# Optimization experiments

Hardware: AMD Instinct MI355X
Metric: run time of the kernel (lower is better)

The kernel has to match this reference:

```python
import jax, jax.numpy as jnp
import numpy as np


def setup_inputs() -> dict:
    key = jax.random.key(0)
    k1, k2, k3, k4 = jax.random.split(key, 4)
    B, S, E, H = 8, 2048, 1024, 64
    x = jax.random.normal(k1, (B, S, E), dtype=jnp.float32)
    # nn.Linear(E, H, bias=False) weight is (H, E); we store transposed (E, H)
    scale = 1.0 / np.sqrt(E)
    Wk = jax.random.normal(k2, (E, H), dtype=jnp.float32) * scale
    Wq = jax.random.normal(k3, (E, H), dtype=jnp.float32) * scale
    Wv = jax.random.normal(k4, (E, H), dtype=jnp.float32) * scale
    return {"x": x, "Wk": Wk, "Wq": Wq, "Wv": Wv}


def reference(x, Wk, Wq, Wv):
    # x: (B, S, E); projections: (B, S, H)
    k = x @ Wk
    q = x @ Wq
    v = x @ Wv
    H = k.shape[-1]
    # scores: (B, S, S) with 1/sqrt(H) scaling as in the torch code
    scores = jnp.einsum("bqh,bkh->bqk", q, k) * (H ** -0.5)
    S = x.shape[1]
    causal = jnp.triu(jnp.full((S, S), -jnp.inf, dtype=scores.dtype), k=1)
    wei = jax.nn.softmax(scores + causal, axis=-1)
    # dropout p=0.0 -> identity
    return jnp.einsum("bqk,bkh->bqh", wei, v)
```

## Files before the change

kernel.cpp:

```cpp
#include <hip/hip_runtime.h>
#include <hip/hip_bf16.h>

typedef unsigned short ushort_t;
typedef __attribute__((ext_vector_type(8))) short short8;
typedef __attribute__((ext_vector_type(4))) short short4v;
typedef __attribute__((ext_vector_type(4))) float f32x4;

__device__ __forceinline__ float bf2f(ushort_t u) {
    unsigned int x = ((unsigned int)u) << 16;
    float f; __builtin_memcpy(&f, &x, 4); return f;
}
__device__ __forceinline__ ushort_t f2bf(float f) {
    __hip_bfloat16 h = __float2bfloat16(f);
    ushort_t u; __builtin_memcpy(&u, &h, 2); return u;
}
__device__ __forceinline__ unsigned packbf2(float a, float b) {
    return (unsigned)f2bf(a) | ((unsigned)f2bf(b) << 16);
}

__device__ __forceinline__ void gload16(const void* g, void* l) {
    __builtin_amdgcn_global_load_lds(
        (const __attribute__((address_space(1))) unsigned int*)g,
        (__attribute__((address_space(3))) unsigned int*)l, 16, 0, 0);
}

constexpr int E  = 1024;
constexpr int Hd = 64;
constexpr int S  = 2048;
constexpr int ROWS = 8 * 2048;
constexpr int NTOT = 192;
constexpr int LSTA = 88;

__global__ __launch_bounds__(256)
void prep_wt(const float* __restrict__ Wk, const float* __restrict__ Wq,
             const float* __restrict__ Wv, ushort_t* __restrict__ WT)
{
    int idx = blockIdx.x * 256 + threadIdx.x;
    int n = idx >> 10;
    int kk = idx & 1023;
    const float* W = (n < 64) ? Wq : ((n < 128) ? Wk : Wv);
    int h = n & 63;
    WT[idx] = f2bf(W[kk * Hd + h]);
}

__global__ __launch_bounds__(256, 2)
void proj_v11(const float* __restrict__ x, const ushort_t* __restrict__ WT,
              ushort_t* __restrict__ qo, ushort_t* __restrict__ ko,
              ushort_t* __restrict__ vTo)
{
    __shared__ alignas(16) float    XS[2][32 * 64];
    __shared__ alignas(16) ushort_t WS[2][192 * 64];

    const int t    = threadIdx.x;
    const int w    = t >> 6;
    const int lane = t & 63;
    const int m    = lane & 15;
    const int g    = lane >> 4;
    const int rl   = m & 7;
    const int rb   = blockIdx.x * 32;

    f32x4 accq[2], acck[2], accv[2];
    #pragma unroll
    for (int j = 0; j < 2; ++j) {
        accq[j] = (f32x4){0.f, 0.f, 0.f, 0.f};
        acck[j] = (f32x4){0.f, 0.f, 0.f, 0.f};
        accv[j] = (f32x4){0.f, 0.f, 0.f, 0.f};
    }

    const int xrow0 = t >> 4;
    const int xrow1 = (256 + t) >> 4;
    const int xU0   = (t & 15) ^ (xrow0 & 7);
    const int xU1   = (t & 15) ^ (xrow1 & 7);
    const float* xs0 = x + (size_t)(rb + xrow0) * E + xU0 * 4;
    const float* xs1 = x + (size_t)(rb + xrow1) * E + xU1 * 4;

    const ushort_t* wsrc[6];
    #pragma unroll
    for (int j = 0; j < 6; ++j) {
        const int L    = j * 256 + t;
        const int wrow = L >> 3;
        const int wU   = (L & 7) ^ (wrow & 7);
        wsrc[j] = WT + (size_t)wrow * E + wU * 8;
    }

    int xiA[2][2], xiB[2][2];
    #pragma unroll
    for (int h = 0; h < 2; ++h)
        #pragma unroll
        for (int kt = 0; kt < 2; ++kt) {
            const int row = h * 16 + m;
            const int U   = kt * 8 + 2 * g;
            xiA[h][kt] = (row * 16 + (U ^ rl)) * 4;
            xiB[h][kt] = (row * 16 + ((U + 1) ^ rl)) * 4;
        }
    int wiq[2], wik[2], wiv[2];
    #pragma unroll
    for (int kt = 0; kt < 2; ++kt) {
        const int U = kt * 4 + g;
        wiq[kt] = ((      w * 16 + m) * 8 + (U ^ rl)) * 8;
        wik[kt] = ((64  + w * 16 + m) * 8 + (U ^ rl)) * 8;
        wiv[kt] = ((128 + w * 16 + m) * 8 + (U ^ rl)) * 8;
    }

    auto STAGE = [&](int buf, int c) {
        const int k0 = c * 64;
        char* xb = (char*)&XS[buf][0];
        char* wb = (char*)&WS[buf][0];
        gload16(xs0 + k0, xb + (size_t)t * 16);
        gload16(xs1 + k0, xb + (size_t)(256 + t) * 16);
        #pragma unroll
        for (int j = 0; j < 6; ++j)
            gload16(wsrc[j] + k0, wb + (size_t)(j * 256 + t) * 16);
    };

    auto COMPUTE = [&](int buf) {
        #pragma unroll
        for (int kt = 0; kt < 2; ++kt) {
            short8 fq = *(const short8*)&WS[buf][wiq[kt]];
            short8 fk = *(const short8*)&WS[buf][wik[kt]];
            short8 fv = *(const short8*)&WS[buf][wiv[kt]];
            #pragma unroll
            for (int h = 0; h < 2; ++h) {
                float4 A = *(const float4*)&XS[buf][xiA[h][kt]];
                float4 B = *(const float4*)&XS[buf][xiB[h][kt]];
                short8 a;
                {
                    unsigned u4[4];
                    u4[0] = packbf2(A.x, A.y);
                    u4[1] = packbf2(A.z, A.w);
                    u4[2] = packbf2(B.x, B.y);
                    u4[3] = packbf2(B.z, B.w);
                    __builtin_memcpy(&a, u4, 16);
                }
                accq[h] = __builtin_amdgcn_mfma_f32_16x16x32_bf16(a, fq, accq[h], 0, 0, 0);
                acck[h] = __builtin_amdgcn_mfma_f32_16x16x32_bf16(a, fk, acck[h], 0, 0, 0);
                accv[h] = __builtin_amdgcn_mfma_f32_16x16x32_bf16(fv, a, accv[h], 0, 0, 0);
            }
        }
    };

    STAGE(0, 0);
    __syncthreads();

    #pragma unroll 1
    for (int cc = 0; cc < 16; cc += 2) {
        STAGE(1, cc + 1);
        COMPUTE(0);
        __syncthreads();
        if (cc + 2 < 16) STAGE(0, cc + 2);
        COMPUTE(1);
        __syncthreads();
    }

    const int col   = w * 16 + m;
    const int batch = rb >> 11;
    const int seq0  = rb & (S - 1);
    #pragma unroll
    for (int mt = 0; mt < 2; ++mt) {
        const int orow = rb + mt * 16 + g * 4;
        #pragma unroll
        for (int r = 0; r < 4; ++r) {
            qo[(size_t)(orow + r) * Hd + col] = f2bf(accq[mt][r] * 0.125f);
            ko[(size_t)(orow + r) * Hd + col] = f2bf(acck[mt][r]);
        }
    }
    #pragma unroll
    for (int ns = 0; ns < 2; ++ns)
        #pragma unroll
        for (int r = 0; r < 4; ++r) {
            const int h = w * 16 + g * 4 + r;
            vTo[(size_t)batch * Hd * S + (size_t)h * S + seq0 + ns * 16 + m]
                = f2bf(accv[ns][r]);
        }
}

__global__ __launch_bounds__(256)
void attn_part(const ushort_t* __restrict__ q, const ushort_t* __restrict__ k,
               const ushort_t* __restrict__ vT,
               float* __restrict__ lp, ushort_t* __restrict__ op)
{
    const int bi     = blockIdx.x;
    const int parity = bi & 3;
    const int pr     = bi >> 2;
    const int batch  = pr & 7;
    const int tile   = 31 - (pr >> 3);
    const int qs0    = tile * 64;
    const int sidx   = (batch * 32 + tile) * 4 + parity;

    const ushort_t* kb  = k  + (size_t)batch * S * Hd;
    const ushort_t* vTb = vT + (size_t)batch * Hd * S;

    const int t    = threadIdx.x;
    const int w    = t >> 6;
    const int lane = t & 63;
    const int m    = lane & 15;
    const int g    = lane >> 4;

    __shared__ alignas(16) ushort_t KS [64][LSTA];
    __shared__ alignas(16) ushort_t VTS[64][LSTA];

    const ushort_t* qrow = q + (size_t)(batch * S + qs0 + w * 16 + m) * Hd;
    short8 qf0 = *(const short8*)(qrow + g * 8);
    short8 qf1 = *(const short8*)(qrow + 32 + g * 8);

    f32x4 o[4];
    #pragma unroll
    for (int j = 0; j < 4; ++j) o[j] = (f32x4){0.f, 0.f, 0.f, 0.f};
    float lrun = 0.f;
    const int qr = w * 16 + m;

    const int r1 = t >> 3, c16 = (t & 7) * 8;
    uint4 pk0, pk1, pv0, pv1;

    int c = parity;
    if (c <= tile) {
        const int key0 = c * 64;
        const ushort_t* kt_base = kb + (size_t)key0 * Hd;
        pk0 = *(const uint4*)(kt_base + t * 8);
        pk1 = *(const uint4*)(kt_base + (t + 256) * 8);
        pv0 = *(const uint4*)(vTb + (size_t)r1 * S + key0 + c16);
        pv1 = *(const uint4*)(vTb + (size_t)(r1 + 32) * S + key0 + c16);
    }

    for (; c <= tile; c += 4) {
        *(uint4*)&KS [r1][c16]       = pk0;
        *(uint4*)&KS [r1 + 32][c16]  = pk1;
        *(uint4*)&VTS[r1][c16]       = pv0;
        *(uint4*)&VTS[r1 + 32][c16]  = pv1;
        __syncthreads();

        if (c + 4 <= tile) {
            const int key0n = (c + 4) * 64;
            const ushort_t* kt_base = kb + (size_t)key0n * Hd;
            pk0 = *(const uint4*)(kt_base + t * 8);
            pk1 = *(const uint4*)(kt_base + (t + 256) * 8);
            pv0 = *(const uint4*)(vTb + (size_t)r1 * S + key0n + c16);
            pv1 = *(const uint4*)(vTb + (size_t)(r1 + 32) * S + key0n + c16);
        }

        f32x4 sacc[4];
        #pragma unroll
        for (int j = 0; j < 4; ++j) sacc[j] = (f32x4){0.f, 0.f, 0.f, 0.f};
        #pragma unroll
        for (int nt = 0; nt < 4; ++nt) {
            short8 b0 = *(const short8*)&KS[nt * 16 + m][g * 8];
            short8 b1 = *(const short8*)&KS[nt * 16 + m][32 + g * 8];
            sacc[nt] = __builtin_amdgcn_mfma_f32_16x16x32_bf16(b0, qf0, sacc[nt], 0, 0, 0);
            sacc[nt] = __builtin_amdgcn_mfma_f32_16x16x32_bf16(b1, qf1, sacc[nt], 0, 0, 0);
        }

        if (c == tile) {
            #pragma unroll
            for (int nt = 0; nt < 4; ++nt)
                #pragma unroll
                for (int r = 0; r < 4; ++r) {
                    const int keyl = nt * 16 + g * 4 + r;
                    sacc[nt][r] = (keyl > qr) ? 0.f : __expf(sacc[nt][r]);
                }
        } else {
            #pragma unroll
            for (int nt = 0; nt < 4; ++nt)
                #pragma unroll
                for (int r = 0; r < 4; ++r)
                    sacc[nt][r] = __expf(sacc[nt][r]);
        }

        #pragma unroll
        for (int nt = 0; nt < 4; ++nt)
            lrun += (sacc[nt][0] + sacc[nt][1]) + (sacc[nt][2] + sacc[nt][3]);

        unsigned pw0[4], pw1[4];
        #pragma unroll
        for (int s = 0; s < 4; ++s) {
            pw0[s] = packbf2(sacc[s][0], sacc[s][1]);
            pw1[s] = packbf2(sacc[s][2], sacc[s][3]);
        }

        #pragma unroll
        for (int s = 0; s < 4; ++s) {
            short4v pa;
            { unsigned u2[2] = {pw0[s], pw1[s]}; __builtin_memcpy(&pa, u2, 8); }
            #pragma unroll
            for (int nt = 0; nt < 4; ++nt) {
                short4v vb = *(const short4v*)&VTS[nt * 16 + m][s * 16 + g * 4];
                o[nt] = __builtin_amdgcn_mfma_f32_16x16x16bf16_1k(pa, vb, o[nt], 0, 0, 0);
            }
        }
        __syncthreads();
    }

    {
        float ts = lrun;
        ts += __shfl_xor(ts, 16, 64);
        ts += __shfl_xor(ts, 32, 64);
        if (lane < 16) lp[sidx * 64 + w * 16 + m] = ts;
    }
    #pragma unroll
    for (int nt = 0; nt < 4; ++nt)
        #pragma unroll
        for (int r = 0; r < 4; ++r)
            op[(size_t)sidx * 4096 + (w * 16 + g * 4 + r) * 64 + nt * 16 + m]
                = f2bf(o[nt][r]);
}

__global__ __launch_bounds__(256)
void attn_merge(const float* __restrict__ lp, const ushort_t* __restrict__ op,
                float* __restrict__ out)
{
    const int bq    = blockIdx.x;
    const int batch = bq >> 5;
    const int tile  = bq & 31;
    const int s0    = (batch * 32 + tile) * 4;

    const int t   = threadIdx.x;
    const int row = t >> 2;
    const int c16 = (t & 3) * 16;

    float l = 0.f;
    #pragma unroll
    for (int p = 0; p < 4; ++p) l += lp[(s0 + p) * 64 + row];
    const float inv = 1.f / l;

    float acc[16];
    #pragma unroll
    for (int j = 0; j < 16; ++j) acc[j] = 0.f;
    #pragma unroll
    for (int p = 0; p < 4; ++p) {
        short8 a0 = *(const short8*)(op + (size_t)(s0 + p) * 4096 + row * 64 + c16);
        short8 a1 = *(const short8*)(op + (size_t)(s0 + p) * 4096 + row * 64 + c16 + 8);
        #pragma unroll
        for (int j = 0; j < 8; ++j) {
            acc[j]     += bf2f((ushort_t)a0[j]);
            acc[j + 8] += bf2f((ushort_t)a1[j]);
        }
    }
    float* dst = out + (size_t)(batch * S + tile * 64 + row) * Hd + c16;
    #pragma unroll
    for (int j = 0; j < 16; ++j) dst[j] = acc[j] * inv;
}

extern "C" void kernel_launch(void* const* d_in, const int* in_sizes, int n_in,
                              void* d_out, int out_size, void* d_ws, size_t ws_size,
                              hipStream_t stream) {
    const float* x  = (const float*)d_in[0];
    const float* Wk = (const float*)d_in[1];
    const float* Wq = (const float*)d_in[2];
    const float* Wv = (const float*)d_in[3];
    float* out = (float*)d_out;

    ushort_t* qws  = (ushort_t*)d_ws;
    ushort_t* kws  = qws + (size_t)ROWS * Hd;
    ushort_t* vTws = kws + (size_t)ROWS * Hd;
    ushort_t* WT   = vTws + (size_t)ROWS * Hd;
    float*    lpp  = (float*)(WT + (size_t)NTOT * E);
    ushort_t* opp  = (ushort_t*)(lpp + 1024 * 64);

    prep_wt<<<(NTOT * E) / 256, 256, 0, stream>>>(Wk, Wq, Wv, WT);
    proj_v11<<<ROWS / 32, 256, 0, stream>>>(x, WT, qws, kws, vTws);
    attn_part<<<1024, 256, 0, stream>>>(qws, kws, vTws, lpp, opp);
    attn_merge<<<256, 256, 0, stream>>>(lpp, opp, out);
}
```

Measured before the change: 132.3 us.

## Enlarge projection tile to 64 rows with 512 threads and triple-buffered loads

The projection kernel now handles 64 rows per block with 8 waves, two row-halves sharing each weight tile, which halves the weight traffic per row. It also replaces double buffering with a three-stage pipeline using explicit vmcnt waits and raw barriers, so three chunks of loads stay in flight while compute runs. Shared memory grows to about 120 KB per block, which may limit residency to one block per CU. The hand-counted vmcnt values must match the five loads issued per stage.

```diff
diff --git a/kernel.cpp b/kernel.cpp
--- a/kernel.cpp
+++ b/kernel.cpp
@@ -30,6 +30,7 @@
 constexpr int ROWS = 8 * 2048;
 constexpr int NTOT = 192;
 constexpr int LSTA = 88;
+constexpr int BM   = 64;
 
 __global__ __launch_bounds__(256)
 void prep_wt(const float* __restrict__ Wk, const float* __restrict__ Wq,
@@ -43,13 +44,13 @@
     WT[idx] = f2bf(W[kk * Hd + h]);
 }
 
-__global__ __launch_bounds__(256, 2)
-void proj_v11(const float* __restrict__ x, const ushort_t* __restrict__ WT,
+__global__ __launch_bounds__(512, 2)
+void proj_v12(const float* __restrict__ x, const ushort_t* __restrict__ WT,
               ushort_t* __restrict__ qo, ushort_t* __restrict__ ko,
               ushort_t* __restrict__ vTo)
 {
-    __shared__ alignas(16) float    XS[2][32 * 64];
-    __shared__ alignas(16) ushort_t WS[2][192 * 64];
+    __shared__ alignas(16) float    XS[3][BM * 64];
+    __shared__ alignas(16) ushort_t WS[3][192 * 64];
 
     const int t    = threadIdx.x;
     const int w    = t >> 6;
@@ -57,7 +58,9 @@
     const int m    = lane & 15;
     const int g    = lane >> 4;
     const int rl   = m & 7;
-    const int rb   = blockIdx.x * 32;
+    const int cg   = w & 3;
+    const int mh   = w >> 2;
+    const int rb   = blockIdx.x * BM;
 
     f32x4 accq[2], acck[2], accv[2];
     #pragma unroll
@@ -67,20 +70,18 @@
         accv[j] = (f32x4){0.f, 0.f, 0.f, 0.f};
     }
 
-    const int xrow0 = t >> 4;
-    const int xrow1 = (256 + t) >> 4;
-    const int xU0   = (t & 15) ^ (xrow0 & 7);
-    const int xU1   = (t & 15) ^ (xrow1 & 7);
-    const float* xs0 = x + (size_t)(rb + xrow0) * E + xU0 * 4;
-    const float* xs1 = x + (size_t)(rb + xrow1) * E + xU1 * 4;
-
-    const ushort_t* wsrc[6];
-    #pragma unroll
-    for (int j = 0; j < 6; ++j) {
-        const int L    = j * 256 + t;
-        const int wrow = L >> 3;
-        const int wU   = (L & 7) ^ (wrow & 7);
-        wsrc[j] = WT + (size_t)wrow * E + wU * 8;
+    const int xr0 = t >> 4,         xu0 = (t & 15) ^ (xr0 & 7);
+    const int xr1 = (t + 512) >> 4, xu1 = (t & 15) ^ (xr1 & 7);
+    const float* xsrc0 = x + (size_t)(rb + xr0) * E + xu0 * 4;
+    const float* xsrc1 = x + (size_t)(rb + xr1) * E + xu1 * 4;
+
+    const ushort_t* wsrc[3];
+    #pragma unroll
+    for (int j = 0; j < 3; ++j) {
+        const int L  = j * 512 + t;
+        const int wr = L >> 3;
+        const int wu = (L & 7) ^ (wr & 7);
+        wsrc[j] = WT + (size_t)wr * E + wu * 8;
     }
 
     int xiA[2][2], xiB[2][2];
@@ -88,7 +89,7 @@
     for (int h = 0; h < 2; ++h)
         #pragma unroll
         for (int kt = 0; kt < 2; ++kt) {
-            const int row = h * 16 + m;
+            const int row = mh * 32 + h * 16 + m;
             const int U   = kt * 8 + 2 * g;
             xiA[h][kt] = (row * 16 + (U ^ rl)) * 4;
             xiB[h][kt] = (row * 16 + ((U + 1) ^ rl)) * 4;
@@ -97,20 +98,20 @@
     #pragma unroll
     for (int kt = 0; kt < 2; ++kt) {
         const int U = kt * 4 + g;
-        wiq[kt] = ((      w * 16 + m) * 8 + (U ^ rl)) * 8;
-        wik[kt] = ((64  + w * 16 + m) * 8 + (U ^ rl)) * 8;
-        wiv[kt] = ((128 + w * 16 + m) * 8 + (U ^ rl)) * 8;
+        wiq[kt] = ((      cg * 16 + m) * 8 + (U ^ rl)) * 8;
+        wik[kt] = ((64  + cg * 16 + m) * 8 + (U ^ rl)) * 8;
+        wiv[kt] = ((128 + cg * 16 + m) * 8 + (U ^ rl)) * 8;
     }
 
     auto STAGE = [&](int buf, int c) {
         const int k0 = c * 64;
         char* xb = (char*)&XS[buf][0];
         char* wb = (char*)&WS[buf][0];
-        gload16(xs0 + k0, xb + (size_t)t * 16);
-        gload16(xs1 + k0, xb + (size_t)(256 + t) * 16);
-        #pragma unroll
-        for (int j = 0; j < 6; ++j)
-            gload16(wsrc[j] + k0, wb + (size_t)(j * 256 + t) * 16);
+        gload16(xsrc0 + k0, xb + (size_t)t * 16);
+        gload16(xsrc1 + k0, xb + (size_t)(t + 512) * 16);
+        #pragma unroll
+        for (int j = 0; j < 3; ++j)
+            gload16(wsrc[j] + k0, wb + (size_t)(j * 512 + t) * 16);
     };
 
     auto COMPUTE = [&](int buf) {
@@ -140,36 +141,39 @@
     };
 
     STAGE(0, 0);
-    __syncthreads();
-
-    #pragma unroll 1
-    for (int cc = 0; cc < 16; cc += 2) {
-        STAGE(1, cc + 1);
-        COMPUTE(0);
-        __syncthreads();
-        if (cc + 2 < 16) STAGE(0, cc + 2);
-        COMPUTE(1);
-        __syncthreads();
-    }
-
-    const int col   = w * 16 + m;
+    STAGE(1, 1);
+    STAGE(2, 2);
+
+    #pragma unroll
+    for (int i = 0; i < 16; ++i) {
+        if (i < 14)       { asm volatile("s_waitcnt vmcnt(10)" ::: "memory"); }
+        else if (i == 14) { asm volatile("s_waitcnt vmcnt(5)"  ::: "memory"); }
+        else              { asm volatile("s_waitcnt vmcnt(0)"  ::: "memory"); }
+        __builtin_amdgcn_sched_barrier(0);
+        __builtin_amdgcn_s_barrier();
+        COMPUTE(i % 3);
+        __builtin_amdgcn_s_barrier();
+        if (i + 3 < 16) STAGE(i % 3, i + 3);
+    }
+
+    const int col   = cg * 16 + m;
     const int batch = rb >> 11;
     const int seq0  = rb & (S - 1);
     #pragma unroll
-    for (int mt = 0; mt < 2; ++mt) {
-        const int orow = rb + mt * 16 + g * 4;
+    for (int h = 0; h < 2; ++h) {
+        const int orow = rb + mh * 32 + h * 16 + g * 4;
         #pragma unroll
         for (int r = 0; r < 4; ++r) {
-            qo[(size_t)(orow + r) * Hd + col] = f2bf(accq[mt][r] * 0.125f);
-            ko[(size_t)(orow + r) * Hd + col] = f2bf(acck[mt][r]);
+            qo[(size_t)(orow + r) * Hd + col] = f2bf(accq[h][r] * 0.125f);
+            ko[(size_t)(orow + r) * Hd + col] = f2bf(acck[h][r]);
         }
     }
     #pragma unroll
     for (int ns = 0; ns < 2; ++ns)
         #pragma unroll
         for (int r = 0; r < 4; ++r) {
-            const int h = w * 16 + g * 4 + r;
-            vTo[(size_t)batch * Hd * S + (size_t)h * S + seq0 + ns * 16 + m]
+            const int hc = cg * 16 + g * 4 + r;
+            vTo[(size_t)batch * Hd * S + (size_t)hc * S + seq0 + mh * 32 + ns * 16 + m]
                 = f2bf(accv[ns][r]);
         }
 }
@@ -356,7 +360,7 @@
     ushort_t* opp  = (ushort_t*)(lpp + 1024 * 64);
 
     prep_wt<<<(NTOT * E) / 256, 256, 0, stream>>>(Wk, Wq, Wv, WT);
-    proj_v11<<<ROWS / 32, 256, 0, stream>>>(x, WT, qws, kws, vTws);
+    proj_v12<<<ROWS / BM, 512, 0, stream>>>(x, WT, qws, kws, vTws);
     attn_part<<<1024, 256, 0, stream>>>(qws, kws, vTws, lpp, opp);
     attn_merge<<<256, 256, 0, stream>>>(lpp, opp, out);
 }
```

Result: faster. 129.0 us (-2.5%).
